# Optimization experiments

Hardware: AMD Instinct MI355X
Metric: run time of the kernel (lower is better)

Reference implementation:

```python
import jax, jax.numpy as jnp
import numpy as np

BOX = 5  # box_size (odd)
PATTERN_SCALE = 16.0


def setup_inputs() -> dict:
    key = jax.random.key(0)
    k1, k2 = jax.random.split(key)
    x = jax.random.normal(k1, (1, 1, 480, 640), dtype=jnp.float32)
    # buffer: uniform in [-pattern_scale, pattern_scale], shape [num_pairs, 2, 2]
    pair_offsets = (jax.random.uniform(k2, (256, 2, 2), dtype=jnp.float32) - 0.5) * 2.0 * PATTERN_SCALE
    return {"x": x, "pair_offsets": pair_offsets}


def _box_average(x, box):
    # replicate-pad then stride-1 average pool => same-size box average
    pad = box // 2
    xp = jnp.pad(x, ((0, 0), (0, 0), (pad, pad), (pad, pad)), mode='edge')
    s = jax.lax.reduce_window(xp, 0.0, jax.lax.add,
                              (1, 1, box, box), (1, 1, 1, 1), 'VALID')
    return s / float(box * box)


def _grid_sample_offsets(img_flat, offsets, B, H, W):
    """Bilinear grid_sample with border padding, align_corners=True,
    for per-pair translational grids. img_flat: [B, H*W]; offsets: [P, 2] (dy, dx).
    Returns [B, P, H, W]."""
    scale_y = 2.0 / (H - 1 + 1e-8)
    scale_x = 2.0 / (W - 1 + 1e-8)
    base_y = jnp.linspace(-1.0, 1.0, H, dtype=img_flat.dtype)[None, :, None]  # [1,H,1]
    base_x = jnp.linspace(-1.0, 1.0, W, dtype=img_flat.dtype)[None, None, :]  # [1,1,W]
    gy = base_y + offsets[:, 0, None, None] * scale_y  # [P,H,1]
    gx = base_x + offsets[:, 1, None, None] * scale_x  # [P,1,W]
    # unnormalize (align_corners=True) and clip coords (padding_mode='border')
    py = jnp.clip((gy + 1.0) * 0.5 * (H - 1), 0.0, H - 1.0)  # [P,H,1]
    px = jnp.clip((gx + 1.0) * 0.5 * (W - 1), 0.0, W - 1.0)  # [P,1,W]
    y0 = jnp.floor(py)
    x0 = jnp.floor(px)
    wy = py - y0  # [P,H,1]
    wx = px - x0  # [P,1,W]
    y0i = y0.astype(jnp.int32)
    x0i = x0.astype(jnp.int32)
    y1i = jnp.minimum(y0i + 1, H - 1)
    x1i = jnp.minimum(x0i + 1, W - 1)

    def gather(yi, xi):
        idx = yi * W + xi  # broadcast -> [P,H,W]
        return jnp.take(img_flat, idx, axis=1)  # [B,P,H,W]

    v = (gather(y0i, x0i) * (1.0 - wy) * (1.0 - wx)
         + gather(y0i, x1i) * (1.0 - wy) * wx
         + gather(y1i, x0i) * wy * (1.0 - wx)
         + gather(y1i, x1i) * wy * wx)
    return v


def reference(x, pair_offsets):
    B, C, H, W = x.shape
    box_avg = _box_average(x, BOX)            # [B,1,H,W]
    img_flat = box_avg[:, 0].reshape(B, H * W)
    s1 = _grid_sample_offsets(img_flat, pair_offsets[:, 0, :], B, H, W)
    s2 = _grid_sample_offsets(img_flat, pair_offsets[:, 1, :], B, H, W)
    return s1 - s2  # binarize=False -> raw differences, [B, P, H, W]
```

## Files before the change

### kernel.cpp

```cpp
#include <hip/hip_runtime.h>

#define H 480
#define W 640
#define NP 256
#define HW (H * W)

#define ABLK 135
#define BBLK 120
#define TOTAL_BLK (NP * (ABLK + BBLK))
#define A_TOTAL (NP * ABLK)

__global__ __launch_bounds__(256) void box_avg_kernel(const float* __restrict__ x,
                                                      float* __restrict__ box) {
    int idx = blockIdx.x * 256 + threadIdx.x;
    int i = idx / W;
    int j = idx - i * W;
    float s = 0.f;
#pragma unroll
    for (int dy = -2; dy <= 2; ++dy) {
        int yy = min(max(i + dy, 0), H - 1);
        const float* row = x + yy * W;
#pragma unroll
        for (int dx = -2; dx <= 2; ++dx) {
            int xx = min(max(j + dx, 0), W - 1);
            s += row[xx];
        }
    }
    box[idx] = s * 0.04f;
}

template<int S>
__device__ __forceinline__ void sample8(const float4 Pa, const float4 Qa, const float4 Ra,
                                        const float4 Pb, const float4 Qb, const float4 Rb,
                                        float wx, float wy, float v[8]) {
    const float ca[12] = {Pa.x, Pa.y, Pa.z, Pa.w, Qa.x, Qa.y, Qa.z, Qa.w, Ra.x, Ra.y, Ra.z, Ra.w};
    const float cb[12] = {Pb.x, Pb.y, Pb.z, Pb.w, Qb.x, Qb.y, Qb.z, Qb.w, Rb.x, Rb.y, Rb.z, Rb.w};
#pragma unroll
    for (int k = 0; k < 8; ++k) {
        float ha = fmaf(wx, ca[S + k + 1] - ca[S + k], ca[S + k]);
        float hb = fmaf(wx, cb[S + k + 1] - cb[S + k], cb[S + k]);
        v[k] = fmaf(wy, hb - ha, ha);
    }
}

#define DISPATCH_S(sv, ...)                                  \
    switch (sv) {                                            \
        case 0:  sample8<0>(__VA_ARGS__); break;             \
        case 1:  sample8<1>(__VA_ARGS__); break;             \
        case 2:  sample8<2>(__VA_ARGS__); break;             \
        default: sample8<3>(__VA_ARGS__); break;             \
    }

__global__ __launch_bounds__(256) void bad_desc_kernel(const float* __restrict__ box,
                                                       const float* __restrict__ po,
                                                       float* __restrict__ out) {
    int b = blockIdx.x;
    if (b < A_TOTAL) {
        int p = b / ABLK;
        int t = (b - p * ABLK) * 256 + threadIdx.x;
        int i = t / 72;
        int g = t - i * 72;
        int j = 32 + (g << 3);

        float dy1 = po[p * 4 + 0];
        float dx1 = po[p * 4 + 1];
        float dy2 = po[p * 4 + 2];
        float dx2 = po[p * 4 + 3];

        float fi = (float)i;
        float fj = (float)j;

        float py1 = fminf(fmaxf(fi + dy1, 0.f), (float)(H - 1));
        int   ya0 = (int)py1;
        float wy1 = py1 - (float)ya0;
        int   ya1 = min(ya0 + 1, H - 1);

        float xf1 = fj + dx1;
        float fl1 = floorf(xf1);
        int   x01 = (int)fl1;
        float wx1 = xf1 - fl1;
        int   s1  = __builtin_amdgcn_readfirstlane(x01 & 3);
        int   m1  = x01 - (x01 & 3);

        const float4* r1a = (const float4*)(box + ya0 * W + m1);
        const float4* r1b = (const float4*)(box + ya1 * W + m1);
        float4 Pa = r1a[0], Qa = r1a[1], Ra = r1a[2];
        float4 Pb = r1b[0], Qb = r1b[1], Rb = r1b[2];

        float v1[8];
        DISPATCH_S(s1, Pa, Qa, Ra, Pb, Qb, Rb, wx1, wy1, v1);

        float py2 = fminf(fmaxf(fi + dy2, 0.f), (float)(H - 1));
        int   yb0 = (int)py2;
        float wy2 = py2 - (float)yb0;
        int   yb1 = min(yb0 + 1, H - 1);

        float xf2 = fj + dx2;
        float fl2 = floorf(xf2);
        int   x02 = (int)fl2;
        float wx2 = xf2 - fl2;
        int   s2  = __builtin_amdgcn_readfirstlane(x02 & 3);
        int   m2  = x02 - (x02 & 3);

        const float4* r2a = (const float4*)(box + yb0 * W + m2);
        const float4* r2b = (const float4*)(box + yb1 * W + m2);
        float4 Pc = r2a[0], Qc = r2a[1], Rc = r2a[2];
        float4 Pd = r2b[0], Qd = r2b[1], Rd = r2b[2];

        float v2[8];
        DISPATCH_S(s2, Pc, Qc, Rc, Pd, Qd, Rd, wx2, wy2, v2);

        float* o = out + ((size_t)p * HW + (size_t)i * W + (size_t)j);
        float4 o0 = {v1[0] - v2[0], v1[1] - v2[1], v1[2] - v2[2], v1[3] - v2[3]};
        float4 o1 = {v1[4] - v2[4], v1[5] - v2[5], v1[6] - v2[6], v1[7] - v2[7]};
        *(float4*)(o)     = o0;
        *(float4*)(o + 4) = o1;
    } else {
        int b2 = b - A_TOTAL;
        int p = b2 / BBLK;
        int t = (b2 - p * BBLK) * 256 + threadIdx.x;
        int i = t >> 6;
        int c = t & 63;
        int j = (c < 32) ? c : 576 + c;

        float dy1 = po[p * 4 + 0];
        float dx1 = po[p * 4 + 1];
        float dy2 = po[p * 4 + 2];
        float dx2 = po[p * 4 + 3];

        float fi = (float)i;
        float fj = (float)j;

        float py1 = fminf(fmaxf(fi + dy1, 0.f), (float)(H - 1));
        int   ya0 = (int)py1;
        float wy1 = py1 - (float)ya0;
        int   ya1 = min(ya0 + 1, H - 1);
        const float* r1a = box + ya0 * W;
        const float* r1b = box + ya1 * W;

        float px = fminf(fmaxf(fj + dx1, 0.f), (float)(W - 1));
        int   x0 = (int)px;
        float wx = px - (float)x0;
        int   x1 = min(x0 + 1, W - 1);
        float a0 = r1a[x0], a1 = r1a[x1];
        float b0 = r1b[x0], b1 = r1b[x1];
        float h0 = fmaf(wx, a1 - a0, a0);
        float h1 = fmaf(wx, b1 - b0, b0);
        float v1 = fmaf(wy1, h1 - h0, h0);

        float py2 = fminf(fmaxf(fi + dy2, 0.f), (float)(H - 1));
        int   yb0 = (int)py2;
        float wy2 = py2 - (float)yb0;
        int   yb1 = min(yb0 + 1, H - 1);
        const float* r2a = box + yb0 * W;
        const float* r2b = box + yb1 * W;

        float qx = fminf(fmaxf(fj + dx2, 0.f), (float)(W - 1));
        int   u0 = (int)qx;
        float ux = qx - (float)u0;
        int   u1 = min(u0 + 1, W - 1);
        float c0 = r2a[u0], c1 = r2a[u1];
        float d0 = r2b[u0], d1 = r2b[u1];
        float g0 = fmaf(ux, c1 - c0, c0);
        float g1 = fmaf(ux, d1 - d0, d0);
        float v2 = fmaf(wy2, g1 - g0, g0);

        out[(size_t)p * HW + (size_t)i * W + (size_t)j] = v1 - v2;
    }
}

extern "C" void kernel_launch(void* const* d_in, const int* in_sizes, int n_in,
                              void* d_out, int out_size, void* d_ws, size_t ws_size,
                              hipStream_t stream) {
    const float* x  = (const float*)d_in[0];
    const float* po = (const float*)d_in[1];
    float* out = (float*)d_out;
    float* box = (float*)d_ws;

    box_avg_kernel<<<HW / 256, 256, 0, stream>>>(x, box);
    bad_desc_kernel<<<TOTAL_BLK, 256, 0, stream>>>(box, po, out);
}
```

Before: 375.0 us.

## Process 8-row bands per thread, reusing horizontal lerps across vertical neighbors

The interior path now has each thread compute an 8-row by 8-column strip. It loads 9 rows instead of 16 and carries the horizontal interpolation of the previous row into the next output row. Rows near the top and bottom edges, where vertical clamping applies, move to a separate per-row path, and column indices are clamped for safety. This cuts redundant box-image loads and lerp arithmetic per output, at the cost of fewer threads, a serial inner loop, and more register pressure.

```diff
diff --git a/kernel.cpp b/kernel.cpp
--- a/kernel.cpp
+++ b/kernel.cpp
@@ -5,10 +5,13 @@
 #define NP 256
 #define HW (H * W)
 
-#define ABLK 135
-#define BBLK 120
-#define TOTAL_BLK (NP * (ABLK + BBLK))
-#define A_TOTAL (NP * ABLK)
+#define P1_BLK 16
+#define P2_BLK 9
+#define P3_BLK 120
+
+#define P1_TOTAL (NP * P1_BLK)
+#define P2_TOTAL (NP * (P1_BLK + P2_BLK))
+#define TOTAL_BLK (NP * (P1_BLK + P2_BLK + P3_BLK))
 
 __global__ __launch_bounds__(256) void box_avg_kernel(const float* __restrict__ x,
                                                       float* __restrict__ box) {
@@ -30,95 +33,173 @@
 }
 
 template<int S>
-__device__ __forceinline__ void sample8(const float4 Pa, const float4 Qa, const float4 Ra,
-                                        const float4 Pb, const float4 Qb, const float4 Rb,
-                                        float wx, float wy, float v[8]) {
-    const float ca[12] = {Pa.x, Pa.y, Pa.z, Pa.w, Qa.x, Qa.y, Qa.z, Qa.w, Ra.x, Ra.y, Ra.z, Ra.w};
-    const float cb[12] = {Pb.x, Pb.y, Pb.z, Pb.w, Qb.x, Qb.y, Qb.z, Qb.w, Rb.x, Rb.y, Rb.z, Rb.w};
-#pragma unroll
-    for (int k = 0; k < 8; ++k) {
-        float ha = fmaf(wx, ca[S + k + 1] - ca[S + k], ca[S + k]);
-        float hb = fmaf(wx, cb[S + k + 1] - cb[S + k], cb[S + k]);
-        v[k] = fmaf(wy, hb - ha, ha);
-    }
-}
-
-#define DISPATCH_S(sv, ...)                                  \
-    switch (sv) {                                            \
-        case 0:  sample8<0>(__VA_ARGS__); break;             \
-        case 1:  sample8<1>(__VA_ARGS__); break;             \
-        case 2:  sample8<2>(__VA_ARGS__); break;             \
-        default: sample8<3>(__VA_ARGS__); break;             \
+__device__ __forceinline__ void hlerp8(const float4 P, const float4 Q, const float4 R,
+                                       float wx, float h[8]) {
+    const float c[12] = {P.x, P.y, P.z, P.w, Q.x, Q.y, Q.z, Q.w, R.x, R.y, R.z, R.w};
+#pragma unroll
+    for (int k = 0; k < 8; ++k)
+        h[k] = fmaf(wx, c[S + k + 1] - c[S + k], c[S + k]);
+}
+
+#define DISPATCH_H(sv, ...)                              \
+    switch (sv) {                                        \
+        case 0:  hlerp8<0>(__VA_ARGS__); break;          \
+        case 1:  hlerp8<1>(__VA_ARGS__); break;          \
+        case 2:  hlerp8<2>(__VA_ARGS__); break;          \
+        default: hlerp8<3>(__VA_ARGS__); break;          \
     }
 
 __global__ __launch_bounds__(256) void bad_desc_kernel(const float* __restrict__ box,
                                                        const float* __restrict__ po,
                                                        float* __restrict__ out) {
     int b = blockIdx.x;
-    if (b < A_TOTAL) {
-        int p = b / ABLK;
-        int t = (b - p * ABLK) * 256 + threadIdx.x;
-        int i = t / 72;
-        int g = t - i * 72;
-        int j = 32 + (g << 3);
+    if (b < P1_TOTAL) {
+        int p = b >> 4;
+        int t = ((b - (p << 4)) << 8) + threadIdx.x;
+        int band = t / 72;
+        if (band >= 56) return;
+        int g = t - band * 72;
+        int i0 = 16 + (band << 3);
+        int j  = 32 + (g << 3);
 
         float dy1 = po[p * 4 + 0];
         float dx1 = po[p * 4 + 1];
         float dy2 = po[p * 4 + 2];
         float dx2 = po[p * 4 + 3];
 
-        float fi = (float)i;
         float fj = (float)j;
-
-        float py1 = fminf(fmaxf(fi + dy1, 0.f), (float)(H - 1));
-        int   ya0 = (int)py1;
-        float wy1 = py1 - (float)ya0;
-        int   ya1 = min(ya0 + 1, H - 1);
 
         float xf1 = fj + dx1;
         float fl1 = floorf(xf1);
         int   x01 = (int)fl1;
         float wx1 = xf1 - fl1;
         int   s1  = __builtin_amdgcn_readfirstlane(x01 & 3);
-        int   m1  = x01 - (x01 & 3);
-
-        const float4* r1a = (const float4*)(box + ya0 * W + m1);
-        const float4* r1b = (const float4*)(box + ya1 * W + m1);
-        float4 Pa = r1a[0], Qa = r1a[1], Ra = r1a[2];
-        float4 Pb = r1b[0], Qb = r1b[1], Rb = r1b[2];
-
-        float v1[8];
-        DISPATCH_S(s1, Pa, Qa, Ra, Pb, Qb, Rb, wx1, wy1, v1);
-
-        float py2 = fminf(fmaxf(fi + dy2, 0.f), (float)(H - 1));
-        int   yb0 = (int)py2;
-        float wy2 = py2 - (float)yb0;
-        int   yb1 = min(yb0 + 1, H - 1);
+        int   m1  = min(max(x01 - (x01 & 3), 0), W - 12);
 
         float xf2 = fj + dx2;
         float fl2 = floorf(xf2);
         int   x02 = (int)fl2;
         float wx2 = xf2 - fl2;
         int   s2  = __builtin_amdgcn_readfirstlane(x02 & 3);
-        int   m2  = x02 - (x02 & 3);
+        int   m2  = min(max(x02 - (x02 & 3), 0), W - 12);
+
+        float fdy1 = floorf(dy1);
+        float wy1  = dy1 - fdy1;
+        int   rA   = min(max(i0 + (int)fdy1, 0), H - 9);
+        float fdy2 = floorf(dy2);
+        float wy2  = dy2 - fdy2;
+        int   rB   = min(max(i0 + (int)fdy2, 0), H - 9);
+
+        const float* baseA = box + rA * W + m1;
+        const float* baseB = box + rB * W + m2;
+
+        float h1p[8], h2p[8], h1c[8], h2c[8];
+        {
+            const float4* ra = (const float4*)baseA;
+            const float4* rb = (const float4*)baseB;
+            float4 Pa = ra[0], Qa = ra[1], Ra = ra[2];
+            float4 Pb = rb[0], Qb = rb[1], Rb = rb[2];
+            DISPATCH_H(s1, Pa, Qa, Ra, wx1, h1p);
+            DISPATCH_H(s2, Pb, Qb, Rb, wx2, h2p);
+        }
+
+        float* o = out + ((size_t)p * HW + (size_t)i0 * W + (size_t)j);
+        for (int k = 1; k <= 8; ++k) {
+            const float4* ra = (const float4*)(baseA + k * W);
+            const float4* rb = (const float4*)(baseB + k * W);
+            float4 Pa = ra[0], Qa = ra[1], Ra = ra[2];
+            float4 Pb = rb[0], Qb = rb[1], Rb = rb[2];
+            DISPATCH_H(s1, Pa, Qa, Ra, wx1, h1c);
+            DISPATCH_H(s2, Pb, Qb, Rb, wx2, h2c);
+
+            float v[8];
+#pragma unroll
+            for (int q = 0; q < 8; ++q) {
+                float a = fmaf(wy1, h1c[q] - h1p[q], h1p[q]);
+                float c = fmaf(wy2, h2c[q] - h2p[q], h2p[q]);
+                v[q] = a - c;
+                h1p[q] = h1c[q];
+                h2p[q] = h2c[q];
+            }
+            float4 o0 = {v[0], v[1], v[2], v[3]};
+            float4 o1 = {v[4], v[5], v[6], v[7]};
+            *(float4*)(o)     = o0;
+            *(float4*)(o + 4) = o1;
+            o += W;
+        }
+    } else if (b < P2_TOTAL) {
+        int b2 = b - P1_TOTAL;
+        int p = b2 / P2_BLK;
+        int t = (b2 - p * P2_BLK) * 256 + threadIdx.x;
+        int ii = t / 72;
+        int g  = t - ii * 72;
+        int i  = (ii < 16) ? ii : 448 + ii;
+        int j  = 32 + (g << 3);
+
+        float dy1 = po[p * 4 + 0];
+        float dx1 = po[p * 4 + 1];
+        float dy2 = po[p * 4 + 2];
+        float dx2 = po[p * 4 + 3];
+
+        float fi = (float)i;
+        float fj = (float)j;
+
+        float py1 = fminf(fmaxf(fi + dy1, 0.f), (float)(H - 1));
+        int   ya0 = (int)py1;
+        float wy1 = py1 - (float)ya0;
+        int   ya1 = min(ya0 + 1, H - 1);
+
+        float xf1 = fj + dx1;
+        float fl1 = floorf(xf1);
+        int   x01 = (int)fl1;
+        float wx1 = xf1 - fl1;
+        int   s1  = __builtin_amdgcn_readfirstlane(x01 & 3);
+        int   m1  = min(max(x01 - (x01 & 3), 0), W - 12);
+
+        const float4* r1a = (const float4*)(box + ya0 * W + m1);
+        const float4* r1b = (const float4*)(box + ya1 * W + m1);
+        float4 Pa = r1a[0], Qa = r1a[1], Ra = r1a[2];
+        float4 Pb = r1b[0], Qb = r1b[1], Rb = r1b[2];
+        float ha[8], hb[8];
+        DISPATCH_H(s1, Pa, Qa, Ra, wx1, ha);
+        DISPATCH_H(s1, Pb, Qb, Rb, wx1, hb);
+
+        float py2 = fminf(fmaxf(fi + dy2, 0.f), (float)(H - 1));
+        int   yb0 = (int)py2;
+        float wy2 = py2 - (float)yb0;
+        int   yb1 = min(yb0 + 1, H - 1);
+
+        float xf2 = fj + dx2;
+        float fl2 = floorf(xf2);
+        int   x02 = (int)fl2;
+        float wx2 = xf2 - fl2;
+        int   s2  = __builtin_amdgcn_readfirstlane(x02 & 3);
+        int   m2  = min(max(x02 - (x02 & 3), 0), W - 12);
 
         const float4* r2a = (const float4*)(box + yb0 * W + m2);
         const float4* r2b = (const float4*)(box + yb1 * W + m2);
         float4 Pc = r2a[0], Qc = r2a[1], Rc = r2a[2];
         float4 Pd = r2b[0], Qd = r2b[1], Rd = r2b[2];
-
-        float v2[8];
-        DISPATCH_S(s2, Pc, Qc, Rc, Pd, Qd, Rd, wx2, wy2, v2);
-
+        float hc[8], hd[8];
+        DISPATCH_H(s2, Pc, Qc, Rc, wx2, hc);
+        DISPATCH_H(s2, Pd, Qd, Rd, wx2, hd);
+
+        float v[8];
+#pragma unroll
+        for (int q = 0; q < 8; ++q) {
+            float a = fmaf(wy1, hb[q] - ha[q], ha[q]);
+            float c = fmaf(wy2, hd[q] - hc[q], hc[q]);
+            v[q] = a - c;
+        }
         float* o = out + ((size_t)p * HW + (size_t)i * W + (size_t)j);
-        float4 o0 = {v1[0] - v2[0], v1[1] - v2[1], v1[2] - v2[2], v1[3] - v2[3]};
-        float4 o1 = {v1[4] - v2[4], v1[5] - v2[5], v1[6] - v2[6], v1[7] - v2[7]};
+        float4 o0 = {v[0], v[1], v[2], v[3]};
+        float4 o1 = {v[4], v[5], v[6], v[7]};
         *(float4*)(o)     = o0;
         *(float4*)(o + 4) = o1;
     } else {
-        int b2 = b - A_TOTAL;
-        int p = b2 / BBLK;
-        int t = (b2 - p * BBLK) * 256 + threadIdx.x;
+        int b2 = b - P2_TOTAL;
+        int p = b2 / P3_BLK;
+        int t = (b2 - p * P3_BLK) * 256 + threadIdx.x;
         int i = t >> 6;
         int c = t & 63;
         int j = (c < 32) ? c : 576 + c;
```

Result: faster. 342.7 us (-8.6%).
